# Performance work log

Hardware: AMD Instinct MI355X
Metric: run time of the kernel (lower is better)

The kernel has to match this reference:

```python
import jax, jax.numpy as jnp
import numpy as np

B, S, J, L, E, H, NI, NT = 8, 32, 4, 32, 500, 500, 5000, 48


def _lstm_scan(x, h0, c0, Wi, Wh, b):
    # x: [T, ..., E]; torch LSTM gate order i,f,g,o
    def step(carry, xt):
        h, c = carry
        z = xt @ Wi.T + h @ Wh.T + b
        i, f, g, o = jnp.split(z, 4, axis=-1)
        c = jax.nn.sigmoid(f) * c + jax.nn.sigmoid(i) * jnp.tanh(g)
        h = jax.nn.sigmoid(o) * jnp.tanh(c)
        return (h, c), h
    (h, c), hs = jax.lax.scan(step, (h0, c0), x)
    return hs, (h, c)


def setup_inputs() -> dict:
    key = jax.random.key(0)
    ks = jax.random.split(key, 24)
    p = lambda k, shp: jax.random.normal(k, shp, jnp.float32) * 0.05
    t = jnp.arange(S)
    return dict(
        item_vectors=jax.random.randint(ks[0], (B, S), 0, NI),
        sequence_tim=jax.random.randint(ks[1], (B, S), 0, NT),
        dilated_idx=jax.random.randint(ks[2], (B, S), 0, S) % jnp.maximum(t, 1)[None, :],
        hist_items=jax.random.randint(ks[3], (B, J, L), 0, NI),
        hist_tims=jax.random.randint(ks[4], (B, J, L), 0, NT),
        mask=jnp.ones((B, S), jnp.float32),
        tim_sim=jax.random.uniform(ks[5], (NT, NT)),
        poi_dist=jax.random.uniform(ks[6], (NI, NI)) + 0.1,
        emb_W=p(ks[7], (NI, E)),
        lstm_Wi=p(ks[8], (4 * H, E)), lstm_Wh=p(ks[9], (4 * H, H)), lstm_b=jnp.zeros((4 * H,)),
        hist_Wi=p(ks[10], (4 * H, E)), hist_Wh=p(ks[11], (4 * H, H)), hist_b=jnp.zeros((4 * H,)),
        dil_Wi=p(ks[12], (4 * H, E)), dil_Wh=p(ks[13], (4 * H, H)), dil_b=jnp.zeros((4 * H,)),
        lin1_W=p(ks[14], (H, H)), lin1_b=jnp.zeros((H,)),
        lin_W=p(ks[15], (NI, 2 * H)), lin_b=jnp.zeros((NI,)),
    )


def _fwd(item_vectors, sequence_tim, dilated_idx, hist_items, hist_tims, mask,
         tim_sim, poi_dist, emb_W, lstm_Wi, lstm_Wh, lstm_b, hist_Wi, hist_Wh,
         hist_b, dil_Wi, dil_Wh, dil_b, lin1_W, lin1_b, lin_W, lin_b):
    items = emb_W[item_vectors]                                  # [B,S,E]
    hs, _ = _lstm_scan(items.transpose(1, 0, 2), jnp.zeros((B, H)), jnp.zeros((B, H)),
                       lstm_Wi, lstm_Wh, lstm_b)
    out = hs.transpose(1, 0, 2)                                  # [B,S,H]

    def dilated_one(xb, idx):
        # dilated LSTMCell: prev state gathered from data-dependent index (zeros at t=0)
        def step(carry, inp):
            Hs, Cs = carry
            t, it, xt = inp
            ph = jnp.where(t == 0, jnp.zeros((H,)), Hs[it])
            pc = jnp.where(t == 0, jnp.zeros((H,)), Cs[it])
            z = xt @ dil_Wi.T + ph @ dil_Wh.T + dil_b
            i, f, g, o = jnp.split(z, 4)
            c = jax.nn.sigmoid(f) * pc + jax.nn.sigmoid(i) * jnp.tanh(g)
            h = jax.nn.sigmoid(o) * jnp.tanh(c)
            return (Hs.at[t].set(h), Cs.at[t].set(c)), None
        (Hs, _), _ = jax.lax.scan(step, (jnp.zeros((S, H)), jnp.zeros((S, H))),
                                  (jnp.arange(S), idx, xb))
        return Hs
    out_hie = jax.vmap(dilated_one)(items, dilated_idx)          # [B,S,H]

    # train-branch session representation: masked mean, same at every step
    denom = jnp.sum(mask, axis=1, keepdims=True)
    pooled = jnp.sum(out * mask[:, :, None], axis=1) / denom     # [B,H]
    csr = jnp.broadcast_to(pooled[:, None, :], (B, S - 1, H))

    def hist_one(items_j, tims_j, timid, poiid, csr_b, out_b):
        jac_rows = tim_sim[timid]                                # [S-1,NT]
        dist_rows = poi_dist[poiid]                              # [S-1,NI]
        def sess_step(carry, inp):
            h2, c2 = carry
            itms, tms = inp
            he, (h2, c2) = _lstm_scan(emb_W[itms], h2, c2, hist_Wi, hist_Wh, hist_b)
            w = jax.nn.softmax(jac_rows[:, tms], axis=1)         # [S-1,L]
            sess_rep = w @ he                                    # [S-1,H]
            avg_d = jnp.mean(dist_rows[:, itms], axis=1)         # [S-1]
            return (h2, c2), (sess_rep, avg_d)
        _, (sess, avgd) = jax.lax.scan(sess_step, (jnp.zeros((H,)), jnp.zeros((H,))),
                                       (items_j, tims_j))
        sess_t = sess.transpose(1, 0, 2)                         # [S-1,J,H]
        avgd_t = avgd.T                                          # [S-1,J]
        sims = jax.nn.softmax(jnp.einsum('sjh,sh->sj', sess_t, csr_b), axis=1)
        out_y = jax.nn.selu(jnp.einsum('sj,sjh->sh', sims, sess_t) @ lin1_W.T + lin1_b)
        layer2 = 0.5 * out_y + 0.5 * out_b[:S - 1]
        l2s = jax.nn.softmax(jnp.einsum('sjh,sh->sj', sess_t, layer2) / avgd_t, axis=1)
        ol2 = jnp.einsum('sj,sjh->sh', l2s, sess_t)              # [S-1,H]
        return jnp.concatenate([ol2, jnp.zeros((1, H))], axis=0)  # pad to [S,H]

    y = jax.nn.selu(jax.vmap(hist_one)(hist_items, hist_tims, sequence_tim[:, :S - 1],
                                       item_vectors[:, :S - 1], csr, out))
    out_mix = 0.5 * (jax.nn.selu(out) + jax.nn.selu(out_hie))
    logits = jnp.concatenate([y, out_mix], axis=2) @ lin_W.T + lin_b
    return jax.nn.log_softmax(logits, axis=-1)


def reference(item_vectors, sequence_tim, dilated_idx, hist_items, hist_tims, mask,
              tim_sim, poi_dist, emb_W, lstm_Wi, lstm_Wh, lstm_b, hist_Wi, hist_Wh,
              hist_b, dil_Wi, dil_Wh, dil_b, lin1_W, lin1_b, lin_W, lin_b):
    return _fwd(item_vectors, sequence_tim, dilated_idx, hist_items, hist_tims, mask,
                tim_sim, poi_dist, emb_W, lstm_Wi, lstm_Wh, lstm_b, hist_Wi, hist_Wh,
                hist_b, dil_Wi, dil_Wh, dil_b, lin1_W, lin1_b, lin_W, lin_b)
```

## Files before the change

kernel.cpp:

```cpp
#include <hip/hip_runtime.h>
#include <hip/hip_bf16.h>
#include <math.h>

#define B_ 8
#define S_ 32
#define J_ 4
#define L_ 32
#define E_ 500
#define H_ 500
#define NI_ 5000
#define NT_ 48
#define G4_ 2000

#define FPAD_ 32

typedef unsigned long long ull;

__device__ __forceinline__ float sigm(float x) { return 1.f / (1.f + expf(-x)); }
__device__ __forceinline__ float seluf(float x) {
    const float sc = 1.0507009873554805f, al = 1.6732632423543772f;
    return x > 0.f ? sc * x : sc * al * (expf(x) - 1.f);
}
__device__ __forceinline__ float cohload(const float* p) {
    return __hip_atomic_load(p, __ATOMIC_RELAXED, __HIP_MEMORY_SCOPE_AGENT);
}
__device__ __forceinline__ ull cohload64(const ull* p) {
    return __hip_atomic_load(p, __ATOMIC_RELAXED, __HIP_MEMORY_SCOPE_AGENT);
}
__device__ __forceinline__ void cohstore(float* p, float v) {
    __hip_atomic_store(p, v, __ATOMIC_RELAXED, __HIP_MEMORY_SCOPE_AGENT);
}

__global__ void k_zero(int* p, int n) {
    int i = blockIdx.x * blockDim.x + threadIdx.x;
    if (i < n) __hip_atomic_store(&p[i], 0, __ATOMIC_RELAXED, __HIP_MEMORY_SCOPE_AGENT);
}

__global__ __launch_bounds__(128) void k_embed(const int* __restrict__ itemv,
                                               const int* __restrict__ histi,
                                               const float* __restrict__ embW,
                                               float* __restrict__ items,
                                               float* __restrict__ histemb) {
    int row = blockIdx.x;
    int id;
    float* dst;
    if (row < 256) { id = itemv[row]; dst = items + (size_t)row * E_; }
    else           { int rr = row - 256; id = histi[rr]; dst = histemb + (size_t)rr * E_; }
    const float4* s = (const float4*)(embW + (size_t)id * E_);
    float4* d = (float4*)dst;
    if (threadIdx.x < 125) d[threadIdx.x] = s[threadIdx.x];
}

#define TBM 64
#define TBN 64
#define TBK 16
__global__ __launch_bounds__(256) void k_gemm_bt(const float* __restrict__ A,
                                                 const float* __restrict__ Bm,
                                                 const float* __restrict__ bias,
                                                 float* __restrict__ C,
                                                 int M, int N, int K) {
    __shared__ float As[TBK][TBM + 1];
    __shared__ float Bs[TBK][TBN + 1];
    const int tid = threadIdx.x;
    const int tx = tid & 15, ty = tid >> 4;
    const int row0 = blockIdx.y * TBM, col0 = blockIdx.x * TBN;
    float acc[4][4] = {};
    for (int k0 = 0; k0 < K; k0 += TBK) {
#pragma unroll
        for (int i = 0; i < 4; ++i) {
            int e = tid + i * 256;
            int kk = e & 15, m = e >> 4;
            int gk = k0 + kk;
            float va = 0.f, vb = 0.f;
            int gm = row0 + m, gn = col0 + m;
            if (gk < K) {
                if (gm < M) va = A[(size_t)gm * K + gk];
                if (gn < N) vb = Bm[(size_t)gn * K + gk];
            }
            As[kk][m] = va;
            Bs[kk][m] = vb;
        }
        __syncthreads();
#pragma unroll
        for (int kk = 0; kk < TBK; ++kk) {
            float a[4], bb[4];
#pragma unroll
            for (int i = 0; i < 4; ++i) a[i] = As[kk][ty * 4 + i];
#pragma unroll
            for (int i = 0; i < 4; ++i) bb[i] = Bs[kk][tx * 4 + i];
#pragma unroll
            for (int i = 0; i < 4; ++i)
#pragma unroll
                for (int j = 0; j < 4; ++j) acc[i][j] += a[i] * bb[j];
        }
        __syncthreads();
    }
#pragma unroll
    for (int i = 0; i < 4; ++i) {
        int gm = row0 + ty * 4 + i;
        if (gm >= M) continue;
#pragma unroll
        for (int j = 0; j < 4; ++j) {
            int gn = col0 + tx * 4 + j;
            if (gn < N) C[(size_t)gm * N + gn] = acc[i][j] + (bias ? bias[gn] : 0.f);
        }
    }
}

__global__ __launch_bounds__(256) void k_rec9(
    const float* __restrict__ xwm, const float* __restrict__ Whm,
    const float* __restrict__ xwd, const float* __restrict__ Whd,
    const int* __restrict__ dilidx,
    const float* __restrict__ xwh, const float* __restrict__ Whh,
    float* __restrict__ outm, float* __restrict__ outh,
    float* __restrict__ csg, float* __restrict__ he,
    int* __restrict__ flags) {
    __shared__ __align__(16) float4 h_s4[125];
    __shared__ float z_s[256];
    const int tid = threadIdx.x;
    const int bid = blockIdx.x;
    const int x = bid & 7, ii = bid >> 3;
    int role, b, blk, K;
    if (x < 4)      { role = 2; b = x * 2 + (ii >> 4);       blk = ii & 15; K = 16; }
    else if (x < 6) { role = 0; b = (x - 4) * 4 + (ii >> 3); blk = ii & 7;  K = 8; }
    else            { role = 1; b = (x - 6) * 4 + (ii >> 3); blk = ii & 7;  K = 8; }

    const int hpbb   = (role == 2) ? 32 : 63;
    const int r0     = blk * hpbb;
    const int hpb    = min(hpbb, 500 - r0);
    const int C      = 4 * hpb;
    const int nsteps = (role == 2) ? 128 : 32;

    const float* Wh = (role == 0) ? Whm : (role == 1) ? Whd : Whh;
    const float* xw = (role == 0) ? xwm : (role == 1) ? xwd : xwh;
    int* flag = flags + (role * 8 + b) * 16 * FPAD_;

    int colg = 0;
    if (tid < C) {
        int gate = tid / hpb;
        int ri = tid - gate * hpb;
        colg = gate * 500 + r0 + ri;
    }
    const float4* wp4 = (const float4*)(Wh + (size_t)colg * 500);

    float c_reg = 0.f;

    for (int t = 0; t < nsteps; ++t) {
        float acc = 0.f;
        if (tid < C) acc = xw[((size_t)(b * nsteps + t)) * G4_ + colg];

        float pc_r = 0.f;
        if (t > 0) {
            if (tid < 64) {
                while (true) {
                    int v = (tid < K)
                        ? __hip_atomic_load(&flag[tid * FPAD_], __ATOMIC_RELAXED,
                                            __HIP_MEMORY_SCOPE_AGENT)
                        : 0x7fffffff;
                    if (__all(v >= t)) break;
                    __builtin_amdgcn_s_sleep(1);
                }
            }
            __syncthreads();

            const float* hrow;
            if (role == 0)      hrow = outm + ((size_t)(b * S_ + (t - 1))) * H_;
            else if (role == 2) hrow = he + ((size_t)(b * 128 + (t - 1))) * H_;
            else { int it = dilidx[b * S_ + t];
                   hrow = outh + ((size_t)(b * S_ + it)) * H_; }
            if (tid < 125) {
                const ull* p = (const ull*)(hrow + tid * 4);
                ull u0 = cohload64(p);
                ull u1 = cohload64(p + 1);
                union { ull u[2]; float4 f; } uf;
                uf.u[0] = u0; uf.u[1] = u1;
                h_s4[tid] = uf.f;
            }
            if (role == 1 && tid < hpb) {
                int it = dilidx[b * S_ + t];
                pc_r = cohload(&csg[((size_t)(b * S_ + it)) * H_ + r0 + tid]);
            }
            __syncthreads();

            if (tid < C) {
                float s0 = 0.f, s1 = 0.f, s2 = 0.f, s3 = 0.f;
#pragma unroll 2
                for (int k4 = 0; k4 < 124; k4 += 4) {
                    float4 w0 = wp4[k4],     h0 = h_s4[k4];
                    float4 w1 = wp4[k4 + 1], h1 = h_s4[k4 + 1];
                    float4 w2 = wp4[k4 + 2], h2 = h_s4[k4 + 2];
                    float4 w3 = wp4[k4 + 3], h3 = h_s4[k4 + 3];
                    s0 += w0.x * h0.x + w0.y * h0.y + w0.z * h0.z + w0.w * h0.w;
                    s1 += w1.x * h1.x + w1.y * h1.y + w1.z * h1.z + w1.w * h1.w;
                    s2 += w2.x * h2.x + w2.y * h2.y + w2.z * h2.z + w2.w * h2.w;
                    s3 += w3.x * h3.x + w3.y * h3.y + w3.z * h3.z + w3.w * h3.w;
                }
                float4 wt = wp4[124], ht = h_s4[124];
                s0 += wt.x * ht.x + wt.y * ht.y + wt.z * ht.z + wt.w * ht.w;
                acc += (s0 + s1) + (s2 + s3);
            }
        }
        z_s[tid] = acc;
        __syncthreads();

        if (tid < hpb) {
            float zi = z_s[tid];
            float zf = z_s[tid + hpb];
            float zg = z_s[tid + 2 * hpb];
            float zo = z_s[tid + 3 * hpb];
            float pc = (role == 1) ? pc_r : c_reg;
            float cc = sigm(zf) * pc + sigm(zi) * tanhf(zg);
            float hh = sigm(zo) * tanhf(cc);
            c_reg = cc;
            int r = r0 + tid;
            if (role == 0) {
                cohstore(&outm[((size_t)(b * S_ + t)) * H_ + r], hh);
            } else if (role == 2) {
                cohstore(&he[((size_t)(b * 128 + t)) * H_ + r], hh);
            } else {
                cohstore(&outh[((size_t)(b * S_ + t)) * H_ + r], hh);
                cohstore(&csg[((size_t)(b * S_ + t)) * H_ + r], cc);
            }
        }
        __syncthreads();
        if (tid == 0)
            __hip_atomic_store(&flag[blk * FPAD_], t + 1, __ATOMIC_RELAXED,
                               __HIP_MEMORY_SCOPE_AGENT);
    }
}

__global__ __launch_bounds__(512) void k_pool(const float* __restrict__ outm,
                                              const float* __restrict__ mask,
                                              float* __restrict__ pooled) {
    int b = blockIdx.x, tid = threadIdx.x;
    if (tid >= 500) return;
    float acc = 0.f, den = 0.f;
    for (int s = 0; s < S_; ++s) {
        float mk = mask[b * S_ + s];
        acc += outm[((size_t)(b * S_ + s)) * H_ + tid] * mk;
        den += mk;
    }
    pooled[b * H_ + tid] = acc / den;
}

__global__ __launch_bounds__(512) void k_sess(const int* __restrict__ seqtim,
                                              const int* __restrict__ itemv,
                                              const int* __restrict__ histt,
                                              const int* __restrict__ histi,
                                              const float* __restrict__ timsim,
                                              const float* __restrict__ poid,
                                              const float* __restrict__ he,
                                              float* __restrict__ sess,
                                              float* __restrict__ avgd) {
    int bi = blockIdx.x;
    int s = bi % 31;
    int tmpv = bi / 31;
    int j = tmpv & 3, b = tmpv >> 2;
    __shared__ float w[L_];
    __shared__ float pd[L_];
    __shared__ float stats[1];
    int tid = threadIdx.x;
    int st = seqtim[b * S_ + s];
    if (tid < L_) {
        int ht = histt[(b * J_ + j) * L_ + tid];
        w[tid] = timsim[st * NT_ + ht];
    }
    if (tid >= 64 && tid < 64 + L_) {
        int l = tid - 64;
        int iv = itemv[b * S_ + s];
        pd[l] = poid[(size_t)iv * NI_ + histi[(b * J_ + j) * L_ + l]];
    }
    __syncthreads();
    if (tid == 64) {
        float a = 0.f;
        for (int l = 0; l < L_; ++l) a += pd[l];
        avgd[(b * J_ + j) * 31 + s] = a * (1.f / 32.f);
    }
    if (tid == 0) {
        float m = -1e30f;
        for (int l = 0; l < L_; ++l) m = fmaxf(m, w[l]);
        float sm = 0.f;
        for (int l = 0; l < L_; ++l) { float e = expf(w[l] - m); w[l] = e; sm += e; }
        stats[0] = 1.f / sm;
    }
    __syncthreads();
    if (tid < 500) {
        float inv = stats[0];
        float acc = 0.f;
        const float* hp = he + ((size_t)(b * J_ * L_ + j * L_)) * H_ + tid;
        for (int l = 0; l < L_; ++l) acc += w[l] * inv * hp[(size_t)l * H_];
        sess[((size_t)((b * J_ + j) * 31 + s)) * H_ + tid] = acc;
    }
}

__global__ __launch_bounds__(512) void k_att1(const float* __restrict__ sess,
                                              const float* __restrict__ pooled,
                                              float* __restrict__ att1) {
    int bi = blockIdx.x;
    int s = bi % 31, b = bi / 31;
    __shared__ float vec[H_];
    __shared__ float part[512];
    int tid = threadIdx.x;
    if (tid < 500) vec[tid] = pooled[b * H_ + tid];
    __syncthreads();
    int j = tid >> 7, i = tid & 127;
    const float* sp = sess + ((size_t)((b * J_ + j) * 31 + s)) * H_;
    float acc = 0.f;
    for (int h = i; h < H_; h += 128) acc += sp[h] * vec[h];
    part[tid] = acc;
    __syncthreads();
    for (int off = 64; off > 0; off >>= 1) {
        if (i < off) part[tid] += part[tid + off];
        __syncthreads();
    }
    float d0 = part[0], d1 = part[128], d2 = part[256], d3 = part[384];
    float m = fmaxf(fmaxf(d0, d1), fmaxf(d2, d3));
    float e0 = expf(d0 - m), e1 = expf(d1 - m), e2 = expf(d2 - m), e3 = expf(d3 - m);
    float inv = 1.f / (e0 + e1 + e2 + e3);
    if (tid < 500) {
        const float* s0 = sess + ((size_t)(b * J_ * 31 + s)) * H_ + tid;
        const size_t js = (size_t)31 * H_;
        float r = e0 * inv * s0[0] + e1 * inv * s0[js] + e2 * inv * s0[2 * js] + e3 * inv * s0[3 * js];
        att1[((size_t)(b * 31 + s)) * H_ + tid] = r;
    }
}

__global__ __launch_bounds__(512) void k_att2(const float* __restrict__ sess,
                                              const float* __restrict__ outy,
                                              const float* __restrict__ outm,
                                              const float* __restrict__ avgd,
                                              float* __restrict__ X) {
    int bi = blockIdx.x;
    int s = bi % 31, b = bi / 31;
    __shared__ float vec[H_];
    __shared__ float part[512];
    int tid = threadIdx.x;
    if (tid < 500)
        vec[tid] = 0.5f * seluf(outy[((size_t)(b * 31 + s)) * H_ + tid]) +
                   0.5f * outm[((size_t)(b * S_ + s)) * H_ + tid];
    __syncthreads();
    int j = tid >> 7, i = tid & 127;
    const float* sp = sess + ((size_t)((b * J_ + j) * 31 + s)) * H_;
    float acc = 0.f;
    for (int h = i; h < H_; h += 128) acc += sp[h] * vec[h];
    part[tid] = acc;
    __syncthreads();
    for (int off = 64; off > 0; off >>= 1) {
        if (i < off) part[tid] += part[tid + off];
        __syncthreads();
    }
    float d0 = part[0]   / avgd[(b * J_ + 0) * 31 + s];
    float d1 = part[128] / avgd[(b * J_ + 1) * 31 + s];
    float d2 = part[256] / avgd[(b * J_ + 2) * 31 + s];
    float d3 = part[384] / avgd[(b * J_ + 3) * 31 + s];
    float m = fmaxf(fmaxf(d0, d1), fmaxf(d2, d3));
    float e0 = expf(d0 - m), e1 = expf(d1 - m), e2 = expf(d2 - m), e3 = expf(d3 - m);
    float inv = 1.f / (e0 + e1 + e2 + e3);
    if (tid < 500) {
        const float* s0 = sess + ((size_t)(b * J_ * 31 + s)) * H_ + tid;
        const size_t js = (size_t)31 * H_;
        float r = e0 * inv * s0[0] + e1 * inv * s0[js] + e2 * inv * s0[2 * js] + e3 * inv * s0[3 * js];
        X[((size_t)(b * S_ + s)) * 1000 + tid] = seluf(r);
    }
}

__global__ __launch_bounds__(512) void k_mix(const float* __restrict__ outm,
                                             const float* __restrict__ outh,
                                             float* __restrict__ X) {
    int bs = blockIdx.x;
    int tid = threadIdx.x;
    if (tid >= 500) return;
    size_t idx = (size_t)bs * H_ + tid;
    float om = 0.5f * (seluf(outm[idx]) + seluf(outh[idx]));
    X[(size_t)bs * 1000 + 500 + tid] = om;
    if ((bs & (S_ - 1)) == S_ - 1) X[(size_t)bs * 1000 + tid] = 0.f;
}

__global__ __launch_bounds__(512) void k_lsm(float* __restrict__ out) {
    int row = blockIdx.x, tid = threadIdx.x;
    float* p = out + (size_t)row * NI_;
    __shared__ float red[512];
    float m = -1e30f;
    for (int i = tid; i < NI_; i += 512) m = fmaxf(m, p[i]);
    red[tid] = m;
    __syncthreads();
    for (int off = 256; off > 0; off >>= 1) {
        if (tid < off) red[tid] = fmaxf(red[tid], red[tid + off]);
        __syncthreads();
    }
    m = red[0];
    __syncthreads();
    float sm = 0.f;
    for (int i = tid; i < NI_; i += 512) sm += expf(p[i] - m);
    red[tid] = sm;
    __syncthreads();
    for (int off = 256; off > 0; off >>= 1) {
        if (tid < off) red[tid] += red[tid + off];
        __syncthreads();
    }
    float lse = m + logf(red[0]);
    __syncthreads();
    for (int i = tid; i < NI_; i += 512) p[i] -= lse;
}

extern "C" void kernel_launch(void* const* d_in, const int* in_sizes, int n_in,
                              void* d_out, int out_size, void* d_ws, size_t ws_size,
                              hipStream_t stream) {
    const int* item_vectors = (const int*)d_in[0];
    const int* sequence_tim = (const int*)d_in[1];
    const int* dilated_idx  = (const int*)d_in[2];
    const int* hist_items   = (const int*)d_in[3];
    const int* hist_tims    = (const int*)d_in[4];
    const float* mask       = (const float*)d_in[5];
    const float* tim_sim    = (const float*)d_in[6];
    const float* poi_dist   = (const float*)d_in[7];
    const float* emb_W      = (const float*)d_in[8];
    const float* lstm_Wi    = (const float*)d_in[9];
    const float* lstm_Wh    = (const float*)d_in[10];
    const float* lstm_b     = (const float*)d_in[11];
    const float* hist_Wi    = (const float*)d_in[12];
    const float* hist_Wh    = (const float*)d_in[13];
    const float* hist_b     = (const float*)d_in[14];
    const float* dil_Wi     = (const float*)d_in[15];
    const float* dil_Wh     = (const float*)d_in[16];
    const float* dil_b      = (const float*)d_in[17];
    const float* lin1_W     = (const float*)d_in[18];
    const float* lin1_b     = (const float*)d_in[19];
    const float* lin_W      = (const float*)d_in[20];
    const float* lin_b      = (const float*)d_in[21];
    float* out = (float*)d_out;
    float* ws  = (float*)d_ws;

    float* items   = ws + 0;
    float* histemb = ws + 128000;
    float* xwm     = ws + 640000;
    float* xwd     = ws + 1152000;
    float* xwh     = ws + 1664000;
    float* outm    = ws + 3712000;
    float* outh    = ws + 3840000;
    float* csg     = ws + 3968000;
    float* he      = ws + 4096000;
    float* pooled  = ws + 4608000;
    float* sess    = ws + 4612000;
    float* avgd    = ws + 5108000;
    float* att1    = ws + 5108992;
    float* outy    = ws + 5232992;
    float* Xbuf    = ws + 5356992;
    int*   flags   = (int*)(ws + 5612992);

    k_zero<<<dim3(48), dim3(256), 0, stream>>>(flags, 24 * 16 * FPAD_);
    k_embed<<<dim3(1280), dim3(128), 0, stream>>>(item_vectors, hist_items, emb_W, items, histemb);

    k_gemm_bt<<<dim3(32, 4), dim3(256), 0, stream>>>(items, lstm_Wi, lstm_b, xwm, 256, G4_, E_);
    k_gemm_bt<<<dim3(32, 4), dim3(256), 0, stream>>>(items, dil_Wi, dil_b, xwd, 256, G4_, E_);
    k_gemm_bt<<<dim3(32, 16), dim3(256), 0, stream>>>(histemb, hist_Wi, hist_b, xwh, 1024, G4_, E_);

    k_rec9<<<dim3(256), dim3(256), 0, stream>>>(
        xwm, lstm_Wh, xwd, dil_Wh, dilated_idx, xwh, hist_Wh,
        outm, outh, csg, he, flags);

    k_pool<<<dim3(B_), dim3(512), 0, stream>>>(outm, mask, pooled);
    k_sess<<<dim3(B_ * J_ * 31), dim3(512), 0, stream>>>(sequence_tim, item_vectors, hist_tims,
                                                         hist_items, tim_sim, poi_dist, he, sess, avgd);
    k_att1<<<dim3(B_ * 31), dim3(512), 0, stream>>>(sess, pooled, att1);
    k_gemm_bt<<<dim3(8, 4), dim3(256), 0, stream>>>(att1, lin1_W, lin1_b, outy, 248, H_, H_);
    k_att2<<<dim3(B_ * 31), dim3(512), 0, stream>>>(sess, outy, outm, avgd, Xbuf);
    k_mix<<<dim3(B_ * S_), dim3(512), 0, stream>>>(outm, outh, Xbuf);

    k_gemm_bt<<<dim3(79, 4), dim3(256), 0, stream>>>(Xbuf, lin_W, lin_b, out, 256, NI_, 1000);
    k_lsm<<<dim3(256), dim3(512), 0, stream>>>(out);
}
```

Before: 1.835 ms.

## Replace per-block flag barriers with sentinel-poisoned data polling in recurrent kernel

Measured after the change: 1.892 ms. +3.1%, slower.

```diff
diff --git a/kernel.cpp b/kernel.cpp
--- a/kernel.cpp
+++ b/kernel.cpp
@@ -12,7 +12,8 @@
 #define NT_ 48
 #define G4_ 2000
 
-#define FPAD_ 32
+#define PZH_ 2.0f
+#define PZC_ 1e30f
 
 typedef unsigned long long ull;
 
@@ -31,9 +32,13 @@
     __hip_atomic_store(p, v, __ATOMIC_RELAXED, __HIP_MEMORY_SCOPE_AGENT);
 }
 
-__global__ void k_zero(int* p, int n) {
-    int i = blockIdx.x * blockDim.x + threadIdx.x;
-    if (i < n) __hip_atomic_store(&p[i], 0, __ATOMIC_RELAXED, __HIP_MEMORY_SCOPE_AGENT);
+__global__ __launch_bounds__(256) void k_poison(float* __restrict__ outm,
+                                                float* __restrict__ outh,
+                                                float* __restrict__ csg,
+                                                float* __restrict__ he) {
+    int i = blockIdx.x * 256 + threadIdx.x;
+    if (i < 128000) { outm[i] = PZH_; outh[i] = PZH_; csg[i] = PZC_; }
+    if (i < 512000) he[i] = PZH_;
 }
 
 __global__ __launch_bounds__(128) void k_embed(const int* __restrict__ itemv,
@@ -107,23 +112,22 @@
     }
 }
 
-__global__ __launch_bounds__(256) void k_rec9(
+__global__ __launch_bounds__(256) void k_rec10(
     const float* __restrict__ xwm, const float* __restrict__ Whm,
     const float* __restrict__ xwd, const float* __restrict__ Whd,
     const int* __restrict__ dilidx,
     const float* __restrict__ xwh, const float* __restrict__ Whh,
     float* __restrict__ outm, float* __restrict__ outh,
-    float* __restrict__ csg, float* __restrict__ he,
-    int* __restrict__ flags) {
+    float* __restrict__ csg, float* __restrict__ he) {
     __shared__ __align__(16) float4 h_s4[125];
     __shared__ float z_s[256];
     const int tid = threadIdx.x;
     const int bid = blockIdx.x;
     const int x = bid & 7, ii = bid >> 3;
-    int role, b, blk, K;
-    if (x < 4)      { role = 2; b = x * 2 + (ii >> 4);       blk = ii & 15; K = 16; }
-    else if (x < 6) { role = 0; b = (x - 4) * 4 + (ii >> 3); blk = ii & 7;  K = 8; }
-    else            { role = 1; b = (x - 6) * 4 + (ii >> 3); blk = ii & 7;  K = 8; }
+    int role, b, blk;
+    if (x < 4)      { role = 2; b = x * 2 + (ii >> 4);       blk = ii & 15; }
+    else if (x < 6) { role = 0; b = (x - 4) * 4 + (ii >> 3); blk = ii & 7;  }
+    else            { role = 1; b = (x - 6) * 4 + (ii >> 3); blk = ii & 7;  }
 
     const int hpbb   = (role == 2) ? 32 : 63;
     const int r0     = blk * hpbb;
@@ -133,7 +137,6 @@
 
     const float* Wh = (role == 0) ? Whm : (role == 1) ? Whd : Whh;
     const float* xw = (role == 0) ? xwm : (role == 1) ? xwd : xwh;
-    int* flag = flags + (role * 8 + b) * 16 * FPAD_;
 
     int colg = 0;
     if (tid < C) {
@@ -151,18 +154,6 @@
 
         float pc_r = 0.f;
         if (t > 0) {
-            if (tid < 64) {
-                while (true) {
-                    int v = (tid < K)
-                        ? __hip_atomic_load(&flag[tid * FPAD_], __ATOMIC_RELAXED,
-                                            __HIP_MEMORY_SCOPE_AGENT)
-                        : 0x7fffffff;
-                    if (__all(v >= t)) break;
-                    __builtin_amdgcn_s_sleep(1);
-                }
-            }
-            __syncthreads();
-
             const float* hrow;
             if (role == 0)      hrow = outm + ((size_t)(b * S_ + (t - 1))) * H_;
             else if (role == 2) hrow = he + ((size_t)(b * 128 + (t - 1))) * H_;
@@ -170,15 +161,20 @@
                    hrow = outh + ((size_t)(b * S_ + it)) * H_; }
             if (tid < 125) {
                 const ull* p = (const ull*)(hrow + tid * 4);
-                ull u0 = cohload64(p);
-                ull u1 = cohload64(p + 1);
-                union { ull u[2]; float4 f; } uf;
-                uf.u[0] = u0; uf.u[1] = u1;
+                union { ull u[2]; float4 f; float fs[4]; } uf;
+                while (true) {
+                    uf.u[0] = cohload64(p);
+                    uf.u[1] = cohload64(p + 1);
+                    if (uf.fs[0] != PZH_ && uf.fs[1] != PZH_ &&
+                        uf.fs[2] != PZH_ && uf.fs[3] != PZH_) break;
+                    __builtin_amdgcn_s_sleep(1);
+                }
                 h_s4[tid] = uf.f;
             }
             if (role == 1 && tid < hpb) {
                 int it = dilidx[b * S_ + t];
-                pc_r = cohload(&csg[((size_t)(b * S_ + it)) * H_ + r0 + tid]);
+                const float* pp = &csg[((size_t)(b * S_ + it)) * H_ + r0 + tid];
+                do { pc_r = cohload(pp); } while (pc_r == PZC_);
             }
             __syncthreads();
 
@@ -223,9 +219,6 @@
             }
         }
         __syncthreads();
-        if (tid == 0)
-            __hip_atomic_store(&flag[blk * FPAD_], t + 1, __ATOMIC_RELAXED,
-                               __HIP_MEMORY_SCOPE_AGENT);
     }
 }
 
@@ -446,18 +439,17 @@
     float* att1    = ws + 5108992;
     float* outy    = ws + 5232992;
     float* Xbuf    = ws + 5356992;
-    int*   flags   = (int*)(ws + 5612992);
-
-    k_zero<<<dim3(48), dim3(256), 0, stream>>>(flags, 24 * 16 * FPAD_);
+
+    k_poison<<<dim3(2000), dim3(256), 0, stream>>>(outm, outh, csg, he);
     k_embed<<<dim3(1280), dim3(128), 0, stream>>>(item_vectors, hist_items, emb_W, items, histemb);
 
     k_gemm_bt<<<dim3(32, 4), dim3(256), 0, stream>>>(items, lstm_Wi, lstm_b, xwm, 256, G4_, E_);
     k_gemm_bt<<<dim3(32, 4), dim3(256), 0, stream>>>(items, dil_Wi, dil_b, xwd, 256, G4_, E_);
     k_gemm_bt<<<dim3(32, 16), dim3(256), 0, stream>>>(histemb, hist_Wi, hist_b, xwh, 1024, G4_, E_);
 
-    k_rec9<<<dim3(256), dim3(256), 0, stream>>>(
+    k_rec10<<<dim3(256), dim3(256), 0, stream>>>(
         xwm, lstm_Wh, xwd, dil_Wh, dilated_idx, xwh, hist_Wh,
-        outm, outh, csg, he, flags);
+        outm, outh, csg, he);
 
     k_pool<<<dim3(B_), dim3(512), 0, stream>>>(outm, mask, pooled);
     k_sess<<<dim3(B_ * J_ * 31), dim3(512), 0, stream>>>(sequence_tim, item_vectors, hist_tims,
```
